# Kernel tuning notes

Measured on AMD Instinct MI355X. Metric: run time of the kernel, lower is better.

The kernel has to match this reference:

```python
import jax, jax.numpy as jnp
import numpy as np
from jax import lax

SHIFT_SIZE = 5
PAD = SHIFT_SIZE // 2


def _chunk_shifts(C):
    # torch.chunk(x, 5, dim=1): chunk size = ceil(C/5); shift for chunk i is i - PAD
    csz = -(-C // SHIFT_SIZE)
    return jnp.arange(C) // csz - PAD  # (C,) in [-PAD, PAD]


def _shift_along_h(x, shifts):
    # x: (B,C,H,W). Equivalent of pad+chunk+roll(dim=2)+cat+narrow: per-channel
    # zero-filled shift along H (no wraparound since |shift| <= PAD).
    B, C, H, W = x.shape
    xp = jnp.pad(x, ((0, 0), (0, 0), (PAD, PAD), (0, 0)))
    c_idx = jnp.arange(C)[:, None]              # (C,1)
    h_idx = jnp.arange(H)[None, :] + PAD - shifts[:, None]  # (C,H)
    return xp[:, c_idx, h_idx, :]               # (B,C,H,W)


def _shift_along_w(x, shifts):
    return jnp.swapaxes(_shift_along_h(jnp.swapaxes(x, 2, 3), shifts), 2, 3)


def setup_inputs() -> dict:
    key = jax.random.key(0)
    ks = jax.random.split(key, 7)
    B, H, W, C, hidden = 8, 128, 128, 256, 256
    x = jax.random.normal(ks[0], (B, H * W, C), dtype=jnp.float32)
    w1 = jax.random.normal(ks[1], (hidden, C), dtype=jnp.float32) * 0.02
    b1 = jnp.zeros((hidden,), dtype=jnp.float32)
    fan_out = 3 * 3 * hidden // hidden  # groups = hidden
    dw_w = jax.random.normal(ks[2], (hidden, 1, 3, 3), dtype=jnp.float32) * np.sqrt(2.0 / fan_out)
    dw_b = jnp.zeros((hidden,), dtype=jnp.float32)
    w2 = jax.random.normal(ks[3], (C, hidden), dtype=jnp.float32) * 0.02
    b2 = jnp.zeros((C,), dtype=jnp.float32)
    return {"x": x, "H": H, "W": W, "w1": w1, "b1": b1,
            "dw_w": dw_w, "dw_b": dw_b, "w2": w2, "b2": b2}


def reference(x, H, W, w1, b1, dw_w, dw_b, w2, b2):
    B, N, C = x.shape
    shifts = _chunk_shifts(C)

    # --- shift along H, then fc1 ---
    xn = jnp.reshape(jnp.swapaxes(x, 1, 2), (B, C, H, W))
    x_s = _shift_along_h(xn, shifts)
    x_s = jnp.swapaxes(x_s.reshape(B, C, H * W), 1, 2)   # (B,N,C)
    h = x_s @ w1.T + b1                                  # (B,N,hidden)

    # --- depthwise 3x3 conv ---
    Ch = h.shape[-1]
    himg = jnp.reshape(jnp.swapaxes(h, 1, 2), (B, Ch, H, W))
    himg = lax.conv_general_dilated(
        himg, dw_w, window_strides=(1, 1), padding=((1, 1), (1, 1)),
        feature_group_count=Ch,
        dimension_numbers=("NCHW", "OIHW", "NCHW")) + dw_b[None, :, None, None]
    h = jnp.swapaxes(himg.reshape(B, Ch, H * W), 1, 2)

    h = jax.nn.gelu(h, approximate=False)

    # --- shift along W, then fc2 ---
    hn = jnp.reshape(jnp.swapaxes(h, 1, 2), (B, Ch, H, W))
    h_s = _shift_along_w(hn, _chunk_shifts(Ch))
    h_s = jnp.swapaxes(h_s.reshape(B, Ch, H * W), 1, 2)  # (B,N,hidden)
    out = h_s @ w2.T + b2                                # (B,N,C)
    return out
```

## Files before the change

### kernel.cpp

```cpp
#include <hip/hip_runtime.h>
#include <hip/hip_bf16.h>
#include <math.h>

#define Hc   128
#define Wc   128
#define Cc   256
#define Nc   (Hc * Wc)
#define Bn   8
#define Mtot (Bn * Nc)
#define CSZ  52
#define SPAD 2

typedef unsigned short ushort4v __attribute__((ext_vector_type(4)));
typedef unsigned short ushort8  __attribute__((ext_vector_type(8)));
typedef __bf16         bf16x8   __attribute__((ext_vector_type(8)));
typedef float          f32x4    __attribute__((ext_vector_type(4)));

__device__ __forceinline__ float bf2f(unsigned short u) {
    return __uint_as_float(((unsigned)u) << 16);
}
__device__ __forceinline__ unsigned short f2bf(float f) {
    unsigned u = __float_as_uint(f);
    return (unsigned short)((u + 0x7fffu + ((u >> 16) & 1u)) >> 16);
}
__device__ __forceinline__ unsigned pk2bf(float a, float b) {
    unsigned ua = __float_as_uint(a) + 0x8000u;
    unsigned ub = __float_as_uint(b) + 0x8000u;
    return __builtin_amdgcn_perm(ub, ua, 0x07060302);
}
__device__ __forceinline__ void async16(const void* g, void* l) {
    __builtin_amdgcn_global_load_lds(
        (const __attribute__((address_space(1))) unsigned*)g,
        (__attribute__((address_space(3))) unsigned*)l, 16, 0, 0);
}

#define FENCE(vm) asm volatile("s_waitcnt vmcnt(" #vm ") lgkmcnt(0)\n\ts_barrier" ::: "memory")

__global__ __launch_bounds__(256)
void wprep_kernel(const float* __restrict__ w1, const float* __restrict__ dw_w,
                  unsigned short* __restrict__ w1b, float* __restrict__ dwT)
{
    const int g = blockIdx.x * 256 + threadIdx.x;
    {
        float4 a = *(const float4*)(w1 + (size_t)g * 4);
        ushort4v o = { f2bf(a.x), f2bf(a.y), f2bf(a.z), f2bf(a.w) };
        *(ushort4v*)(w1b + (size_t)g * 4) = o;
    }
    if (g < 9 * Cc) dwT[(g % 9) * Cc + g / 9] = dw_w[g];
}

__global__ __launch_bounds__(256)
void fc1_mfma_kernel(const float* __restrict__ x, const unsigned short* __restrict__ w1b,
                     const float* __restrict__ b1, unsigned short* __restrict__ h1)
{
    __shared__ __align__(16) unsigned char smem[40960];
    __bf16* As = (__bf16*)smem;
    __bf16* Bs = (__bf16*)(smem + 16384);
    unsigned short* Cs = (unsigned short*)smem;

    const int tid  = threadIdx.x;
    const int lane = tid & 63;
    const int wave = tid >> 6;
    const int wm = (wave >> 1) * 64, wn = (wave & 1) * 64;

    const int lid = ((blockIdx.x & 7) << 8) | (blockIdx.x >> 3);
    const int bx  = lid >> 1;
    const int j0  = (lid & 1) * 128;
    const size_t m0 = (size_t)bx * 128;
    const int bb = bx >> 7, hh = bx & 127;
    const int r = tid >> 1, half = tid & 1;
    const int idx0 = tid, idx1 = tid + 256;

    const int xr  = (r >> 2) & 3;
    const int sA0 = ((half * 2 + 0) ^ xr) * 8;
    const int sA1 = ((half * 2 + 1) ^ xr) * 8;
    const int bxo0 = ((idx0 & 3) ^ ((idx0 >> 4) & 3)) * 8;
    const int bxo1 = ((idx1 & 3) ^ ((idx1 >> 4) & 3)) * 8;
    const size_t bro0 = (size_t)(j0 + (idx0 >> 2)) * Cc;
    const size_t bro1 = (size_t)(j0 + (idx1 >> 2)) * Cc;

    float4 av0[4], av1[4];

    auto loadA = [&](int t, float4* av) {
        const int kb = t * 32 + half * 16;
#pragma unroll
        for (int j = 0; j < 4; ++j) {
            const int c  = kb + j * 4;
            const int s  = c / CSZ - SPAD;
            const int hs = hh - s;
            av[j] = make_float4(0.f, 0.f, 0.f, 0.f);
            if (hs >= 0 && hs < Hc)
                av[j] = *(const float4*)(x + ((size_t)(bb * Nc + hs * Wc + r)) * Cc + c);
        }
    };
    auto storeA = [&](int buf, const float4* av) {
        uint4 q0, q1;
        q0.x = pk2bf(av[0].x, av[0].y); q0.y = pk2bf(av[0].z, av[0].w);
        q0.z = pk2bf(av[1].x, av[1].y); q0.w = pk2bf(av[1].z, av[1].w);
        q1.x = pk2bf(av[2].x, av[2].y); q1.y = pk2bf(av[2].z, av[2].w);
        q1.z = pk2bf(av[3].x, av[3].y); q1.w = pk2bf(av[3].z, av[3].w);
        __bf16* base = As + buf * 4096 + r * 32;
        *(uint4*)(base + sA0) = q0;
        *(uint4*)(base + sA1) = q1;
    };
    auto stageB = [&](int buf, int t) {
        const int k0 = t * 32;
        __bf16* bdst = Bs + buf * 4096;
        async16(w1b + bro0 + k0 + bxo0, bdst + idx0 * 8);
        async16(w1b + bro1 + k0 + bxo1, bdst + idx1 * 8);
    };

    f32x4 acc[4][4] = {};
    const int kq  = (lane >> 4) * 8;
    const int kqx = kq ^ (((lane >> 2) & 3) << 3);
    const int rr  = lane & 15;

    loadA(0, av0);
    stageB(0, 0);
    stageB(1, 1);
    loadA(1, av1);
    storeA(0, av0);
    FENCE(6);

#define F1_STEP(T, AVL, AVS, FN)                                              \
    {                                                                          \
        if constexpr ((T) <= 5) { loadA((T) + 2, AVL); stageB(((T) + 2) % 3, (T) + 2); } \
        bf16x8 a[4], b[4];                                                     \
        const __bf16* ap = As + ((T) & 1) * 4096;                              \
        const __bf16* bp = Bs + ((T) % 3) * 4096;                              \
        _Pragma("unroll")                                                      \
        for (int i = 0; i < 4; ++i) {                                          \
            a[i] = *(const bf16x8*)(ap + (wm + i * 16 + rr) * 32 + kqx);       \
            b[i] = *(const bf16x8*)(bp + (wn + i * 16 + rr) * 32 + kqx);       \
        }                                                                      \
        _Pragma("unroll")                                                      \
        for (int i = 0; i < 4; ++i)                                            \
            _Pragma("unroll")                                                  \
            for (int j = 0; j < 4; ++j)                                        \
                acc[i][j] = __builtin_amdgcn_mfma_f32_16x16x32_bf16(a[i], b[j], acc[i][j], 0, 0, 0); \
        if constexpr ((T) <= 6) storeA(((T) + 1) & 1, AVS);                    \
        FN;                                                                    \
    }

    F1_STEP(0, av0, av1, FENCE(6));
    F1_STEP(1, av1, av0, FENCE(6));
    F1_STEP(2, av0, av1, FENCE(6));
    F1_STEP(3, av1, av0, FENCE(6));
    F1_STEP(4, av0, av1, FENCE(6));
    F1_STEP(5, av1, av0, FENCE(6));
    F1_STEP(6, av0, av1, FENCE(0));
    F1_STEP(7, av1, av0, FENCE(0));
#undef F1_STEP

    const int cq = (lane >> 4) * 4;
    const int cc = lane & 15;
    float bv[4];
#pragma unroll
    for (int j = 0; j < 4; ++j) bv[j] = b1[j0 + wn + j * 16 + cc];
#pragma unroll
    for (int i = 0; i < 4; ++i)
#pragma unroll
        for (int j = 0; j < 4; ++j) {
            const int col = wn + j * 16 + cc;
#pragma unroll
            for (int rg = 0; rg < 4; ++rg)
                Cs[(wm + i * 16 + cq + rg) * 136 + col] = f2bf(acc[i][j][rg] + bv[j]);
        }
    __syncthreads();
    {
        const int row = tid >> 1, hf = tid & 1;
        const unsigned short* src = Cs + row * 136 + hf * 64;
        unsigned short* dst = h1 + (m0 + row) * Cc + j0 + hf * 64;
#pragma unroll
        for (int i = 0; i < 8; ++i)
            *(uint4*)(dst + i * 8) = *(const uint4*)(src + i * 8);
    }
}

__global__ __launch_bounds__(256)
void zero_borders_kernel(unsigned short* __restrict__ gsh)
{
    const int gid = blockIdx.x * 256 + threadIdx.x;
    const int cg  = gid & 31;
    const int rest = gid >> 5;
    const int wi = rest & 3;
    const int bh = rest >> 2;
    const int w  = (wi & 2) ? (wi + 124) : wi;
    uint4 z; z.x = z.y = z.z = z.w = 0u;
    *(uint4*)(gsh + ((size_t)bh * 128 + w) * Cc + cg * 8) = z;
}

__global__ __launch_bounds__(256)
void dwconv_gelu_scatter_kernel(const unsigned short* __restrict__ h1,
                                const float* __restrict__ dwT, const float* __restrict__ dw_b,
                                unsigned short* __restrict__ gsh)
{
    const int t   = threadIdx.x;
    const int cg  = t & 31;
    const int wq  = t >> 5;
    const int c0  = cg * 8;
    const int bh  = blockIdx.x >> 2;
    const int qtr = blockIdx.x & 3;
    const int bb  = bh >> 7, hh = bh & 127;
    const size_t rowb = (size_t)bb * Nc + (size_t)hh * Wc;
    const int wbase = qtr * 32 + wq * 4 - 1;

    float acc[4][8];
    {
        float4 a0 = *(const float4*)(dw_b + c0);
        float4 a1 = *(const float4*)(dw_b + c0 + 4);
#pragma unroll
        for (int i = 0; i < 4; ++i) {
            acc[i][0] = a0.x; acc[i][1] = a0.y; acc[i][2] = a0.z; acc[i][3] = a0.w;
            acc[i][4] = a1.x; acc[i][5] = a1.y; acc[i][6] = a1.z; acc[i][7] = a1.w;
        }
    }

#pragma unroll
    for (int dy = -1; dy <= 1; ++dy) {
        const int y = hh + dy;
        if (y < 0 || y >= Hc) continue;
        const unsigned short* rp = h1 + ((size_t)bb * Nc + (size_t)y * Wc) * Cc + c0;
        float in[6][8];
#pragma unroll
        for (int dx = 0; dx < 6; ++dx) {
            const int w = wbase + dx;
            ushort8 raw = {0, 0, 0, 0, 0, 0, 0, 0};
            if (w >= 0 && w < Wc) raw = *(const ushort8*)(rp + (size_t)w * Cc);
#pragma unroll
            for (int c = 0; c < 8; ++c) in[dx][c] = bf2f(raw[c]);
        }
        const float* wrow = dwT + (dy + 1) * 3 * Cc + c0;
        float wr[3][8];
#pragma unroll
        for (int tx = 0; tx < 3; ++tx) {
            float4 wa = *(const float4*)(wrow + tx * Cc);
            float4 wb = *(const float4*)(wrow + tx * Cc + 4);
            wr[tx][0] = wa.x; wr[tx][1] = wa.y; wr[tx][2] = wa.z; wr[tx][3] = wa.w;
            wr[tx][4] = wb.x; wr[tx][5] = wb.y; wr[tx][6] = wb.z; wr[tx][7] = wb.w;
        }
#pragma unroll
        for (int i = 0; i < 4; ++i)
#pragma unroll
            for (int tx = 0; tx < 3; ++tx)
#pragma unroll
                for (int c = 0; c < 8; ++c)
                    acc[i][c] += in[i + tx][c] * wr[tx][c];
    }

    const int s0 = c0 / CSZ - SPAD;
    const int s1 = (c0 + 4) / CSZ - SPAD;
#pragma unroll
    for (int i = 0; i < 4; ++i) {
        float g[8];
#pragma unroll
        for (int c = 0; c < 8; ++c) {
            const float v = acc[i][c];
            const float u = v * v;
            const float a = __builtin_fmaf(0.0713548162f, u, 1.5957691216f);
            const float e = __expf(v * a);
            g[c] = v * e * __builtin_amdgcn_rcpf(e + 1.0f);
        }
        uint2 lo, hi;
        lo.x = pk2bf(g[0], g[1]); lo.y = pk2bf(g[2], g[3]);
        hi.x = pk2bf(g[4], g[5]); hi.y = pk2bf(g[6], g[7]);
        const int wo = wbase + 1 + i;
        const int w0 = wo + s0, w1 = wo + s1;
        if ((unsigned)w0 < (unsigned)Wc) *(uint2*)(gsh + (rowb + w0) * Cc + c0)     = lo;
        if ((unsigned)w1 < (unsigned)Wc) *(uint2*)(gsh + (rowb + w1) * Cc + c0 + 4) = hi;
    }
}

__global__ __launch_bounds__(256)
void fc2_mfma_kernel(const unsigned short* __restrict__ A, const float* __restrict__ w2,
                     const float* __restrict__ b2, float* __restrict__ out)
{
    __shared__ __align__(16) unsigned char smem[40960];
    __bf16* As = (__bf16*)smem;
    __bf16* Bs = (__bf16*)(smem + 24576);

    const int tid  = threadIdx.x;
    const int lane = tid & 63;
    const int wave = tid >> 6;
    const int wm = (wave >> 1) * 64, wn = (wave & 1) * 64;

    const int lid = ((blockIdx.x & 7) << 8) | (blockIdx.x >> 3);
    const size_t m0 = (size_t)(lid >> 1) * 128;
    const int j0 = (lid & 1) * 128;

    const int idx0 = tid, idx1 = tid + 256;
    const int brow = tid >> 1, bhalf = tid & 1;

    const int axo0 = ((idx0 & 3) ^ ((idx0 >> 4) & 3)) * 8;
    const int axo1 = ((idx1 & 3) ^ ((idx1 >> 4) & 3)) * 8;
    const size_t aro0 = (m0 + (idx0 >> 2)) * Cc;
    const size_t aro1 = (m0 + (idx1 >> 2)) * Cc;
    const int xrB = (brow >> 2) & 3;
    const int sB0 = ((bhalf * 2 + 0) ^ xrB) * 8;
    const int sB1 = ((bhalf * 2 + 1) ^ xrB) * 8;

    float4 wv[4];
    auto loadB = [&](int t) {
        const float* src = w2 + (size_t)(j0 + brow) * Cc + t * 32 + bhalf * 16;
        wv[0] = *(const float4*)(src);
        wv[1] = *(const float4*)(src + 4);
        wv[2] = *(const float4*)(src + 8);
        wv[3] = *(const float4*)(src + 12);
    };
    auto storeB = [&](int buf) {
        uint4 p0, p1;
        p0.x = pk2bf(wv[0].x, wv[0].y); p0.y = pk2bf(wv[0].z, wv[0].w);
        p0.z = pk2bf(wv[1].x, wv[1].y); p0.w = pk2bf(wv[1].z, wv[1].w);
        p1.x = pk2bf(wv[2].x, wv[2].y); p1.y = pk2bf(wv[2].z, wv[2].w);
        p1.z = pk2bf(wv[3].x, wv[3].y); p1.w = pk2bf(wv[3].z, wv[3].w);
        __bf16* base = Bs + buf * 4096 + brow * 32;
        *(uint4*)(base + sB0) = p0;
        *(uint4*)(base + sB1) = p1;
    };
    auto stageA = [&](int buf, int t) {
        const int k0 = t * 32;
        __bf16* adst = As + buf * 4096;
        async16(A + aro0 + k0 + axo0, adst + idx0 * 8);
        async16(A + aro1 + k0 + axo1, adst + idx1 * 8);
    };

    f32x4 acc[4][4] = {};
    const int kq  = (lane >> 4) * 8;
    const int kqx = kq ^ (((lane >> 2) & 3) << 3);
    const int rr  = lane & 15;

    loadB(0);
    stageA(0, 0);
    stageA(1, 1);
    storeB(0);
    FENCE(2);

#define F2_STEP(T, FN)                                                        \
    {                                                                          \
        if constexpr ((T) <= 6) loadB((T) + 1);                                \
        if constexpr ((T) <= 5) stageA(((T) + 2) % 3, (T) + 2);                \
        bf16x8 a[4], b[4];                                                     \
        const __bf16* ap = As + ((T) % 3) * 4096;                              \
        const __bf16* bp = Bs + ((T) & 1) * 4096;                              \
        _Pragma("unroll")                                                      \
        for (int i = 0; i < 4; ++i) {                                          \
            a[i] = *(const bf16x8*)(ap + (wm + i * 16 + rr) * 32 + kqx);       \
            b[i] = *(const bf16x8*)(bp + (wn + i * 16 + rr) * 32 + kqx);       \
        }                                                                      \
        _Pragma("unroll")                                                      \
        for (int i = 0; i < 4; ++i)                                            \
            _Pragma("unroll")                                                  \
            for (int j = 0; j < 4; ++j)                                        \
                acc[i][j] = __builtin_amdgcn_mfma_f32_16x16x32_bf16(a[i], b[j], acc[i][j], 0, 0, 0); \
        if constexpr ((T) <= 6) storeB(((T) + 1) & 1);                         \
        FN;                                                                    \
    }

    F2_STEP(0, FENCE(2));
    F2_STEP(1, FENCE(2));
    F2_STEP(2, FENCE(2));
    F2_STEP(3, FENCE(2));
    F2_STEP(4, FENCE(2));
    F2_STEP(5, FENCE(2));
    F2_STEP(6, FENCE(0));
    F2_STEP(7, FENCE(0));
#undef F2_STEP

    const int cq = (lane >> 4) * 4;
    const int cc = lane & 15;
    float bv[4];
#pragma unroll
    for (int j = 0; j < 4; ++j) bv[j] = b2[j0 + wn + j * 16 + cc];
#pragma unroll
    for (int i = 0; i < 4; ++i)
#pragma unroll
        for (int j = 0; j < 4; ++j) {
            const int col = j0 + wn + j * 16 + cc;
#pragma unroll
            for (int rg = 0; rg < 4; ++rg)
                out[(m0 + wm + i * 16 + cq + rg) * Cc + col] = acc[i][j][rg] + bv[j];
        }
}

extern "C" void kernel_launch(void* const* d_in, const int* in_sizes, int n_in,
                              void* d_out, int out_size, void* d_ws, size_t ws_size,
                              hipStream_t stream) {
    const float* x    = (const float*)d_in[0];
    const float* w1   = (const float*)d_in[3];
    const float* b1   = (const float*)d_in[4];
    const float* dw_w = (const float*)d_in[5];
    const float* dw_b = (const float*)d_in[6];
    const float* w2   = (const float*)d_in[7];
    const float* b2   = (const float*)d_in[8];
    float* out = (float*)d_out;

    unsigned short* h1  = (unsigned short*)d_ws;
    unsigned short* gsh = h1 + (size_t)Mtot * Cc;
    unsigned short* w1b = (unsigned short*)d_out;
    float*          dwT = (float*)(w1b + 65536);

    wprep_kernel<<<dim3(64), dim3(256), 0, stream>>>(w1, dw_w, w1b, dwT);
    fc1_mfma_kernel<<<dim3(2 * Mtot / 128), dim3(256), 0, stream>>>(x, w1b, b1, h1);
    zero_borders_kernel<<<dim3(512), dim3(256), 0, stream>>>(gsh);
    dwconv_gelu_scatter_kernel<<<dim3(4 * Mtot / 128), dim3(256), 0, stream>>>(h1, dwT, dw_b, gsh);
    fc2_mfma_kernel<<<dim3(2 * Mtot / 128), dim3(256), 0, stream>>>(gsh, w2, b2, out);
}
```

Measured before the change: 359.5 us.

## Split H-shift and bf16 conversion into a separate pre-pass before fc1

Measured after the change: 357.9 us. No clear change (-0.4%).

```diff
diff --git a/kernel.cpp b/kernel.cpp
--- a/kernel.cpp
+++ b/kernel.cpp
@@ -50,10 +50,30 @@
 }
 
 __global__ __launch_bounds__(256)
-void fc1_mfma_kernel(const float* __restrict__ x, const unsigned short* __restrict__ w1b,
+void shiftcvt_kernel(const float* __restrict__ x, unsigned short* __restrict__ xb)
+{
+    const int gid0 = blockIdx.x * 256 + threadIdx.x;
+#pragma unroll
+    for (int it = 0; it < 4; ++it) {
+        const int gid = gid0 + it * (8192 * 256);
+        const int row = gid >> 6;
+        const int c   = (gid & 63) * 4;
+        const int hh  = (row >> 7) & 127;
+        const int s   = c / CSZ - SPAD;
+        const int hs  = hh - s;
+        float4 v = make_float4(0.f, 0.f, 0.f, 0.f);
+        if (hs >= 0 && hs < Hc)
+            v = *(const float4*)(x + ((size_t)row + (size_t)(hs - hh) * Wc) * Cc + c);
+        uint2 o; o.x = pk2bf(v.x, v.y); o.y = pk2bf(v.z, v.w);
+        *(uint2*)(xb + (size_t)row * Cc + c) = o;
+    }
+}
+
+__global__ __launch_bounds__(256)
+void fc1_mfma_kernel(const unsigned short* __restrict__ xb, const unsigned short* __restrict__ w1b,
                      const float* __restrict__ b1, unsigned short* __restrict__ h1)
 {
-    __shared__ __align__(16) unsigned char smem[40960];
+    __shared__ __align__(16) unsigned char smem[34816];
     __bf16* As = (__bf16*)smem;
     __bf16* Bs = (__bf16*)(smem + 16384);
     unsigned short* Cs = (unsigned short*)smem;
@@ -67,90 +87,50 @@
     const int bx  = lid >> 1;
     const int j0  = (lid & 1) * 128;
     const size_t m0 = (size_t)bx * 128;
-    const int bb = bx >> 7, hh = bx & 127;
-    const int r = tid >> 1, half = tid & 1;
     const int idx0 = tid, idx1 = tid + 256;
 
-    const int xr  = (r >> 2) & 3;
-    const int sA0 = ((half * 2 + 0) ^ xr) * 8;
-    const int sA1 = ((half * 2 + 1) ^ xr) * 8;
-    const int bxo0 = ((idx0 & 3) ^ ((idx0 >> 4) & 3)) * 8;
-    const int bxo1 = ((idx1 & 3) ^ ((idx1 >> 4) & 3)) * 8;
-    const size_t bro0 = (size_t)(j0 + (idx0 >> 2)) * Cc;
-    const size_t bro1 = (size_t)(j0 + (idx1 >> 2)) * Cc;
-
-    float4 av0[4], av1[4];
-
-    auto loadA = [&](int t, float4* av) {
-        const int kb = t * 32 + half * 16;
-#pragma unroll
-        for (int j = 0; j < 4; ++j) {
-            const int c  = kb + j * 4;
-            const int s  = c / CSZ - SPAD;
-            const int hs = hh - s;
-            av[j] = make_float4(0.f, 0.f, 0.f, 0.f);
-            if (hs >= 0 && hs < Hc)
-                av[j] = *(const float4*)(x + ((size_t)(bb * Nc + hs * Wc + r)) * Cc + c);
-        }
+    const size_t aro0 = (m0 + (idx0 >> 2)) * Cc + (idx0 & 3) * 8;
+    const size_t aro1 = (m0 + (idx1 >> 2)) * Cc + (idx1 & 3) * 8;
+    const size_t bro0 = (size_t)(j0 + (idx0 >> 2)) * Cc + (idx0 & 3) * 8;
+    const size_t bro1 = (size_t)(j0 + (idx1 >> 2)) * Cc + (idx1 & 3) * 8;
+
+    auto stage = [&](int buf, int t) {
+        const int k0 = t * 32;
+        __bf16* adst = As + buf * 4096;
+        __bf16* bdst = Bs + buf * 4096;
+        async16(xb  + aro0 + k0, adst + idx0 * 8);
+        async16(xb  + aro1 + k0, adst + idx1 * 8);
+        async16(w1b + bro0 + k0, bdst + idx0 * 8);
+        async16(w1b + bro1 + k0, bdst + idx1 * 8);
     };
-    auto storeA = [&](int buf, const float4* av) {
-        uint4 q0, q1;
-        q0.x = pk2bf(av[0].x, av[0].y); q0.y = pk2bf(av[0].z, av[0].w);
-        q0.z = pk2bf(av[1].x, av[1].y); q0.w = pk2bf(av[1].z, av[1].w);
-        q1.x = pk2bf(av[2].x, av[2].y); q1.y = pk2bf(av[2].z, av[2].w);
-        q1.z = pk2bf(av[3].x, av[3].y); q1.w = pk2bf(av[3].z, av[3].w);
-        __bf16* base = As + buf * 4096 + r * 32;
-        *(uint4*)(base + sA0) = q0;
-        *(uint4*)(base + sA1) = q1;
-    };
-    auto stageB = [&](int buf, int t) {
-        const int k0 = t * 32;
-        __bf16* bdst = Bs + buf * 4096;
-        async16(w1b + bro0 + k0 + bxo0, bdst + idx0 * 8);
-        async16(w1b + bro1 + k0 + bxo1, bdst + idx1 * 8);
-    };
 
     f32x4 acc[4][4] = {};
-    const int kq  = (lane >> 4) * 8;
-    const int kqx = kq ^ (((lane >> 2) & 3) << 3);
-    const int rr  = lane & 15;
-
-    loadA(0, av0);
-    stageB(0, 0);
-    stageB(1, 1);
-    loadA(1, av1);
-    storeA(0, av0);
-    FENCE(6);
-
-#define F1_STEP(T, AVL, AVS, FN)                                              \
-    {                                                                          \
-        if constexpr ((T) <= 5) { loadA((T) + 2, AVL); stageB(((T) + 2) % 3, (T) + 2); } \
-        bf16x8 a[4], b[4];                                                     \
-        const __bf16* ap = As + ((T) & 1) * 4096;                              \
-        const __bf16* bp = Bs + ((T) % 3) * 4096;                              \
-        _Pragma("unroll")                                                      \
-        for (int i = 0; i < 4; ++i) {                                          \
-            a[i] = *(const bf16x8*)(ap + (wm + i * 16 + rr) * 32 + kqx);       \
-            b[i] = *(const bf16x8*)(bp + (wn + i * 16 + rr) * 32 + kqx);       \
-        }                                                                      \
-        _Pragma("unroll")                                                      \
-        for (int i = 0; i < 4; ++i)                                            \
-            _Pragma("unroll")                                                  \
-            for (int j = 0; j < 4; ++j)                                        \
-                acc[i][j] = __builtin_amdgcn_mfma_f32_16x16x32_bf16(a[i], b[j], acc[i][j], 0, 0, 0); \
-        if constexpr ((T) <= 6) storeA(((T) + 1) & 1, AVS);                    \
-        FN;                                                                    \
-    }
-
-    F1_STEP(0, av0, av1, FENCE(6));
-    F1_STEP(1, av1, av0, FENCE(6));
-    F1_STEP(2, av0, av1, FENCE(6));
-    F1_STEP(3, av1, av0, FENCE(6));
-    F1_STEP(4, av0, av1, FENCE(6));
-    F1_STEP(5, av1, av0, FENCE(6));
-    F1_STEP(6, av0, av1, FENCE(0));
-    F1_STEP(7, av1, av0, FENCE(0));
-#undef F1_STEP
+    const int kq = (lane >> 4) * 8;
+    const int rr = lane & 15;
+
+    stage(0, 0);
+    __syncthreads();
+
+    int cur = 0;
+    for (int t = 0; t < 8; ++t) {
+        const int nxt = cur ^ 1;
+        if (t < 7) stage(nxt, t + 1);
+        bf16x8 a[4], b[4];
+        const __bf16* ap = As + cur * 4096;
+        const __bf16* bp = Bs + cur * 4096;
+#pragma unroll
+        for (int i = 0; i < 4; ++i) {
+            a[i] = *(const bf16x8*)(ap + (wm + i * 16 + rr) * 32 + kq);
+            b[i] = *(const bf16x8*)(bp + (wn + i * 16 + rr) * 32 + kq);
+        }
+#pragma unroll
+        for (int i = 0; i < 4; ++i)
+#pragma unroll
+            for (int j = 0; j < 4; ++j)
+                acc[i][j] = __builtin_amdgcn_mfma_f32_16x16x32_bf16(a[i], b[j], acc[i][j], 0, 0, 0);
+        __syncthreads();
+        cur = nxt;
+    }
 
     const int cq = (lane >> 4) * 4;
     const int cc = lane & 15;
@@ -400,7 +380,8 @@
     float*          dwT = (float*)(w1b + 65536);
 
     wprep_kernel<<<dim3(64), dim3(256), 0, stream>>>(w1, dw_w, w1b, dwT);
-    fc1_mfma_kernel<<<dim3(2 * Mtot / 128), dim3(256), 0, stream>>>(x, w1b, b1, h1);
+    shiftcvt_kernel<<<dim3(8192), dim3(256), 0, stream>>>(x, gsh);
+    fc1_mfma_kernel<<<dim3(2 * Mtot / 128), dim3(256), 0, stream>>>(gsh, w1b, b1, h1);
     zero_borders_kernel<<<dim3(512), dim3(256), 0, stream>>>(gsh);
     dwconv_gelu_scatter_kernel<<<dim3(4 * Mtot / 128), dim3(256), 0, stream>>>(h1, dwT, dw_b, gsh);
     fc2_mfma_kernel<<<dim3(2 * Mtot / 128), dim3(256), 0, stream>>>(gsh, w2, b2, out);
```
